# Performance work log

Measured on AMD Instinct MI355X. Metric: run time of the kernel, lower is better.

Reference implementation:

```python
import jax, jax.numpy as jnp
import numpy as np

OBS, ACT, EMB, DET, STO = 512, 32, 1024, 1024, 256
T, B = 64, 256
KL_SCALE = 1.0


def setup_inputs() -> dict:
    key = jax.random.key(0)
    ks = jax.random.split(key, 24)
    s = 0.02
    inp = {
        "obs": jax.random.normal(ks[0], (T, B, OBS), jnp.float32),
        "actions": jax.random.normal(ks[1], (T, B, ACT), jnp.float32),
        "rewards": jax.random.normal(ks[2], (T, B), jnp.float32),
        "dones": jnp.zeros((T, B), jnp.bool_),
        "eps": jax.random.normal(ks[3], (T - 1, B, STO), jnp.float32),
        # encoder: Linear(OBS,EMB) -> ReLU -> Linear(EMB,EMB) -> ReLU
        "enc_w1": jax.random.normal(ks[4], (OBS, EMB)) * s,
        "enc_b1": jnp.zeros((EMB,)),
        "enc_w2": jax.random.normal(ks[5], (EMB, EMB)) * s,
        "enc_b2": jnp.zeros((EMB,)),
        # GRUCell(STO+ACT, DET), torch layout [3*DET, in], gate order r,z,n
        "gru_wih": jax.random.normal(ks[6], (3 * DET, STO + ACT)) * s,
        "gru_whh": jax.random.normal(ks[7], (3 * DET, DET)) * s,
        "gru_bih": jnp.zeros((3 * DET,)),
        "gru_bhh": jnp.zeros((3 * DET,)),
        # prior / posterior nets
        "prior_w": jax.random.normal(ks[8], (DET, 2 * STO)) * s,
        "prior_b": jnp.zeros((2 * STO,)),
        "post_w": jax.random.normal(ks[9], (DET + EMB, 2 * STO)) * s,
        "post_b": jnp.zeros((2 * STO,)),
        # obs decoder
        "dec_w1": jax.random.normal(ks[10], (DET + STO, EMB)) * s,
        "dec_b1": jnp.zeros((EMB,)),
        "dec_w2": jax.random.normal(ks[11], (EMB, OBS)) * s,
        "dec_b2": jnp.zeros((OBS,)),
        # reward head
        "rew_w1": jax.random.normal(ks[12], (DET + STO, EMB)) * s,
        "rew_b1": jnp.zeros((EMB,)),
        "rew_w2": jax.random.normal(ks[13], (EMB, 1)) * s,
        "rew_b2": jnp.zeros((1,)),
    }
    return inp


def _kl(mq, lq, mp, lp):
    vq = jnp.exp(2.0 * lq)
    vp = jnp.exp(2.0 * lp)
    kl = lp - lq + (vq + (mq - mp) ** 2) / (vp + 1e-8) - 1.0
    return 0.5 * jnp.sum(kl, axis=-1)


def reference(obs, actions, rewards, dones, eps,
              enc_w1, enc_b1, enc_w2, enc_b2,
              gru_wih, gru_whh, gru_bih, gru_bhh,
              prior_w, prior_b, post_w, post_b,
              dec_w1, dec_b1, dec_w2, dec_b2,
              rew_w1, rew_b1, rew_w2, rew_b2):
    def step(carry, xs):
        h, z = carry
        o_t, o_next, a_t, r_t, d_t, e_t = xs
        # encoder
        emb = jax.nn.relu(jax.nn.relu(o_t @ enc_w1 + enc_b1) @ enc_w2 + enc_b2)
        # prior / posterior
        pm, pl = jnp.split(h @ prior_w + prior_b, 2, axis=-1)
        qm, ql = jnp.split(jnp.concatenate([h, emb], -1) @ post_w + post_b, 2, axis=-1)
        z_post = qm + e_t * jnp.exp(ql)
        # GRUCell (torch semantics)
        x = jnp.concatenate([z_post, a_t], -1)
        gi = x @ gru_wih.T + gru_bih
        gh = h @ gru_whh.T + gru_bhh
        ir, iz, inn = jnp.split(gi, 3, -1)
        hr, hz, hn = jnp.split(gh, 3, -1)
        r = jax.nn.sigmoid(ir + hr)
        u = jax.nn.sigmoid(iz + hz)
        n = jnp.tanh(inn + r * hn)
        h_next = (1.0 - u) * n + u * h
        feat = jnp.concatenate([h_next, z_post], -1)
        pred_obs = jax.nn.relu(feat @ dec_w1 + dec_b1) @ dec_w2 + dec_b2
        pred_rew = (jax.nn.relu(feat @ rew_w1 + rew_b1) @ rew_w2 + rew_b2)[..., 0]
        recon = jnp.mean((pred_obs - o_next) ** 2, axis=-1)  # [B]
        rew_l = (pred_rew - r_t) ** 2                         # [B]
        kl = _kl(qm, ql, pm, pl)                              # [B]
        mask = 1.0 - d_t.astype(h_next.dtype)[:, None]
        return (h_next * mask, z_post * mask), (recon, rew_l, kl)

    h0 = jnp.zeros((B, DET), obs.dtype)
    z0 = jnp.zeros((B, STO), obs.dtype)
    xs = (obs[:-1], obs[1:], actions[:-1], rewards[:-1], dones[:-1], eps)
    _, (recon, rew_l, kl) = jax.lax.scan(step, (h0, z0), xs)
    recon_loss = jnp.mean(recon)
    reward_loss = jnp.mean(rew_l)
    kl_loss = jnp.mean(kl)
    total = recon_loss + reward_loss + KL_SCALE * kl_loss
    return jnp.stack([total, recon_loss, reward_loss, kl_loss])
```

## Files before the change

kernel.cpp:

```cpp
#include <hip/hip_runtime.h>
#include <math.h>


namespace {

typedef unsigned short ushort;
typedef __attribute__((ext_vector_type(8))) short short8;
typedef __attribute__((ext_vector_type(4))) float f32x4;

constexpr int TSTEPS = 63;
constexpr int NB     = 256;
constexpr int NACT   = 32;
constexpr int NROWS  = TSTEPS * NB;
constexpr int TGRP   = 7;
constexpr int NGRP   = 9;
constexpr int GROWS  = TGRP * NB;

constexpr size_t OFF_POSTE = 0;
constexpr size_t OFF_OBSB  = OFF_POSTE + (size_t)NROWS * 512;
constexpr size_t OFF_E1C   = OFF_OBSB + (size_t)GROWS * 512 / 2;
constexpr size_t OFF_EMBC  = OFF_E1C + (size_t)GROWS * 1024 / 2;
constexpr size_t OFF_FEATC = OFF_EMBC + (size_t)GROWS * 1024 / 2;
constexpr size_t OFF_DR1C  = OFF_FEATC + (size_t)GROWS * 1280 / 2;
constexpr size_t OFF_WHT   = OFF_DR1C + (size_t)GROWS * 2048 / 2;
constexpr size_t OFF_WIHT  = OFF_WHT + (size_t)4096 * 1024 / 2;
constexpr size_t OFF_WDRT  = OFF_WIHT + (size_t)3072 * 288 / 2;
constexpr size_t OFF_E1T   = OFF_WDRT + (size_t)2048 * 1280 / 2;
constexpr size_t OFF_E2T   = OFF_E1T + (size_t)1024 * 512 / 2;
constexpr size_t OFF_PET   = OFF_E2T + (size_t)1024 * 1024 / 2;
constexpr size_t OFF_DW2T  = OFF_PET + (size_t)512 * 1024 / 2;
constexpr size_t OFF_BDR   = OFF_DW2T + (size_t)512 * 1024 / 2;
constexpr size_t OFF_G     = OFF_BDR + 2048;
constexpr size_t OFF_H     = OFF_G + (size_t)NB * 3072;
constexpr size_t OFF_HB    = OFF_H + (size_t)NB * 1024;
constexpr size_t OFF_ACC   = OFF_HB + (size_t)NB * 1024 / 2;
constexpr size_t OFF_XBUF  = OFF_ACC + 16;

__device__ __forceinline__ ushort f2bf(float f) {
  unsigned int u = __float_as_uint(f);
  unsigned int r = (u + 0x7fffu + ((u >> 16) & 1u)) >> 16;
  return (ushort)r;
}
__device__ __forceinline__ float bf2f(ushort u) {
  return __uint_as_float((unsigned int)u << 16);
}

__global__ void zero_kernel(float* p, int n) {
  int i = blockIdx.x * 256 + threadIdx.x;
  if (i < n) p[i] = 0.f;
}

__global__ void f2bf_kernel(const float* __restrict__ in, ushort* __restrict__ out, int n) {
  int i = blockIdx.x * 256 + threadIdx.x;
  if (i < n) out[i] = f2bf(in[i]);
}

__global__ void build_wht(const float* __restrict__ prior_w, const float* __restrict__ post_w,
                          const float* __restrict__ whh, ushort* __restrict__ out) {
  int idx = blockIdx.x * 256 + threadIdx.x;
  int n = idx >> 10, k = idx & 1023;
  float v;
  if (n < 1024) {
    int q = (n >> 4) & 3;
    int s = ((n >> 6) << 4) | (n & 15);
    v = (q == 0) ? prior_w[k * 512 + s]
      : (q == 1) ? prior_w[k * 512 + 256 + s]
      : (q == 2) ? post_w[k * 512 + s]
                 : post_w[k * 512 + 256 + s];
  } else {
    v = whh[(size_t)(n - 1024) * 1024 + k];
  }
  out[idx] = f2bf(v);
}

__global__ void trans_conv(const float* __restrict__ in, ushort* __restrict__ out,
                           int ldi, int ldo) {
  __shared__ float tile[32][33];
  int r0 = blockIdx.y * 32, c0 = blockIdx.x * 32;
  int tx = threadIdx.x & 31, ty = threadIdx.x >> 5;
#pragma unroll
  for (int p = 0; p < 4; ++p)
    tile[ty + p * 8][tx] = in[(size_t)(r0 + ty + p * 8) * ldi + c0 + tx];
  __syncthreads();
#pragma unroll
  for (int p = 0; p < 4; ++p)
    out[(size_t)(c0 + ty + p * 8) * ldo + r0 + tx] = f2bf(tile[tx][ty + p * 8]);
}

__global__ void build_bdr(const float* __restrict__ dec_b1, const float* __restrict__ rew_b1,
                          float* __restrict__ bdr) {
  int i = blockIdx.x * 256 + threadIdx.x;
  bdr[i] = (i < 1024) ? dec_b1[i] : rew_b1[i - 1024];
}

template <int EPI>
__global__ __launch_bounds__(256) void gemm_bf16(
    const ushort* __restrict__ A, const ushort* __restrict__ BT,
    const float* __restrict__ bias, void* __restrict__ Cv,
    int K, int lda, int ldb, int ldc) {
  __shared__ __align__(16) ushort As[64 * 40];
  __shared__ __align__(16) ushort Bs[64 * 40];
  int tid = threadIdx.x;
  int wave = tid >> 6, lane = tid & 63;
  int quad = lane >> 4, l15 = lane & 15;
  int m0 = blockIdx.y * 64, n0 = blockIdx.x * 64;
  int sr = tid >> 2, sc = (tid & 3) * 8;
  f32x4 acc[4] = {};
  for (int k0 = 0; k0 < K; k0 += 32) {
    *(int4*)&As[sr * 40 + sc] = *(const int4*)(A + (size_t)(m0 + sr) * lda + k0 + sc);
    *(int4*)&Bs[sr * 40 + sc] = *(const int4*)(BT + (size_t)(n0 + sr) * ldb + k0 + sc);
    __syncthreads();
    short8 a = *(const short8*)&As[(wave * 16 + l15) * 40 + quad * 8];
#pragma unroll
    for (int c = 0; c < 4; ++c) {
      short8 b = *(const short8*)&Bs[(c * 16 + l15) * 40 + quad * 8];
      acc[c] = __builtin_amdgcn_mfma_f32_16x16x32_bf16(a, b, acc[c], 0, 0, 0);
    }
    __syncthreads();
  }
#pragma unroll
  for (int c = 0; c < 4; ++c) {
#pragma unroll
    for (int r = 0; r < 4; ++r) {
      size_t row = m0 + wave * 16 + quad * 4 + r;
      int col = n0 + c * 16 + l15;
      float v = acc[c][r] + bias[col];
      if (EPI == 1) v = fmaxf(v, 0.f);
      if (EPI == 1) ((ushort*)Cv)[row * ldc + col] = f2bf(v);
      else ((float*)Cv)[row * ldc + col] = v;
    }
  }
}

__global__ __launch_bounds__(256) void step_g_kernel(
    int t, int tt, const ushort* __restrict__ HB, const ushort* __restrict__ WHT,
    const float* __restrict__ prior_b, const float* __restrict__ poste,
    const float* __restrict__ eps, const float* __restrict__ actions,
    float* __restrict__ G, ushort* __restrict__ xbuf,
    ushort* __restrict__ featc, float* __restrict__ acc_kl) {
  __shared__ __align__(16) ushort As[64 * 72];
  __shared__ __align__(16) ushort Bs[64 * 72];
  int tid = threadIdx.x;
  int wave = tid >> 6, lane = tid & 63;
  int quad = lane >> 4, l15 = lane & 15;
  int m0 = blockIdx.y * 64, n0 = blockIdx.x * 64;
  int sr = tid >> 2, sc = (tid & 3) * 16;
  const ushort* agp = HB + (size_t)(m0 + sr) * 1024 + sc;
  const ushort* bgp = WHT + (size_t)(n0 + sr) * 1024 + sc;
  int4 a0 = *(const int4*)agp, a1 = *(const int4*)(agp + 8);
  int4 b0 = *(const int4*)bgp, b1 = *(const int4*)(bgp + 8);
  f32x4 acc[4] = {};
  for (int k0 = 0;;) {
    *(int4*)&As[sr * 72 + sc] = a0; *(int4*)&As[sr * 72 + sc + 8] = a1;
    *(int4*)&Bs[sr * 72 + sc] = b0; *(int4*)&Bs[sr * 72 + sc + 8] = b1;
    __syncthreads();
    int kn = k0 + 64;
    if (kn < 1024) {
      a0 = *(const int4*)(agp + kn); a1 = *(const int4*)(agp + kn + 8);
      b0 = *(const int4*)(bgp + kn); b1 = *(const int4*)(bgp + kn + 8);
    }
#pragma unroll
    for (int kk = 0; kk < 2; ++kk) {
      short8 a = *(const short8*)&As[(wave * 16 + l15) * 72 + kk * 32 + quad * 8];
#pragma unroll
      for (int c = 0; c < 4; ++c) {
        short8 b = *(const short8*)&Bs[(c * 16 + l15) * 72 + kk * 32 + quad * 8];
        acc[c] = __builtin_amdgcn_mfma_f32_16x16x32_bf16(a, b, acc[c], 0, 0, 0);
      }
    }
    k0 = kn;
    if (k0 >= 1024) break;
    __syncthreads();
  }
  if (blockIdx.x < 16) {
    int s = (n0 >> 2) + l15;
    float kl_sum = 0.f;
#pragma unroll
    for (int r = 0; r < 4; ++r) {
      int b = m0 + wave * 16 + quad * 4 + r;
      size_t row = (size_t)t * NB + b;
      float pm = acc[0][r] + prior_b[s];
      float pl = acc[1][r] + prior_b[256 + s];
      float qm = acc[2][r] + poste[row * 512 + s];
      float ql = acc[3][r] + poste[row * 512 + 256 + s];
      float e = eps[row * 256 + s];
      float z = qm + e * expf(ql);
      xbuf[b * 288 + s] = f2bf(z);
      featc[(size_t)(tt * NB + b) * 1280 + 1024 + s] = f2bf(z);
      if (s < NACT) xbuf[b * 288 + 256 + s] = f2bf(actions[row * NACT + s]);
      float vq = expf(2.f * ql), vp = expf(2.f * pl);
      float dm = qm - pm;
      kl_sum += pl - ql + (vq + dm * dm) / (vp + 1e-8f) - 1.f;
    }
    for (int off = 32; off > 0; off >>= 1) kl_sum += __shfl_down(kl_sum, off);
    if (lane == 0) atomicAdd(acc_kl, 0.5f * kl_sum);
  } else {
    int ng = n0 - 1024;
#pragma unroll
    for (int c = 0; c < 4; ++c)
#pragma unroll
      for (int r = 0; r < 4; ++r) {
        int b = m0 + wave * 16 + quad * 4 + r;
        G[(size_t)b * 3072 + ng + c * 16 + l15] = acc[c][r];
      }
  }
}

__global__ __launch_bounds__(256) void gru_step_kernel(
    int t, int tt, const ushort* __restrict__ xbuf, const ushort* __restrict__ wiht,
    const float* __restrict__ G, const float* __restrict__ bih,
    const float* __restrict__ bhh, const unsigned char* __restrict__ dones,
    float* __restrict__ H, ushort* __restrict__ HB, ushort* __restrict__ featc) {
  __shared__ __align__(16) ushort As[64 * 40];
  __shared__ __align__(16) ushort Bs[3][64 * 40];
  int tid = threadIdx.x;
  int wave = tid >> 6, lane = tid & 63;
  int quad = lane >> 4, l15 = lane & 15;
  int m0 = blockIdx.y * 64, n0 = blockIdx.x * 64;
  int sr = tid >> 2, sc = (tid & 3) * 8;
  const ushort* agp = xbuf + (size_t)(m0 + sr) * 288 + sc;
  const ushort* bgp0 = wiht + (size_t)(n0 + sr) * 288 + sc;
  int4 pa = *(const int4*)agp;
  int4 pb0 = *(const int4*)bgp0;
  int4 pb1 = *(const int4*)(bgp0 + (size_t)1024 * 288);
  int4 pb2 = *(const int4*)(bgp0 + (size_t)2048 * 288);
  f32x4 accv[3][4] = {};
  for (int k0 = 0;;) {
    *(int4*)&As[sr * 40 + sc] = pa;
    *(int4*)&Bs[0][sr * 40 + sc] = pb0;
    *(int4*)&Bs[1][sr * 40 + sc] = pb1;
    *(int4*)&Bs[2][sr * 40 + sc] = pb2;
    __syncthreads();
    int kn = k0 + 32;
    if (kn < 288) {
      pa = *(const int4*)(agp + kn);
      pb0 = *(const int4*)(bgp0 + kn);
      pb1 = *(const int4*)(bgp0 + (size_t)1024 * 288 + kn);
      pb2 = *(const int4*)(bgp0 + (size_t)2048 * 288 + kn);
    }
    short8 a = *(const short8*)&As[(wave * 16 + l15) * 40 + quad * 8];
#pragma unroll
    for (int gg = 0; gg < 3; ++gg) {
#pragma unroll
      for (int c = 0; c < 4; ++c) {
        short8 b = *(const short8*)&Bs[gg][(c * 16 + l15) * 40 + quad * 8];
        accv[gg][c] = __builtin_amdgcn_mfma_f32_16x16x32_bf16(a, b, accv[gg][c], 0, 0, 0);
      }
    }
    k0 = kn;
    if (k0 >= 288) break;
    __syncthreads();
  }
#pragma unroll
  for (int c = 0; c < 4; ++c) {
#pragma unroll
    for (int r = 0; r < 4; ++r) {
      int b_idx = m0 + wave * 16 + quad * 4 + r;
      int j = n0 + c * 16 + l15;
      const float* g = G + (size_t)b_idx * 3072;
      float ir = accv[0][c][r] + bih[j];
      float iz = accv[1][c][r] + bih[1024 + j];
      float in_ = accv[2][c][r] + bih[2048 + j];
      float hr = g[j] + bhh[j];
      float hz = g[1024 + j] + bhh[1024 + j];
      float hn = g[2048 + j] + bhh[2048 + j];
      float rg = 1.f / (1.f + expf(-(ir + hr)));
      float u = 1.f / (1.f + expf(-(iz + hz)));
      float n = tanhf(in_ + rg * hn);
      float hprev = H[b_idx * 1024 + j];
      float hnext = (1.f - u) * n + u * hprev;
      featc[(size_t)(tt * NB + b_idx) * 1280 + j] = f2bf(hnext);
      float mask = 1.f - (float)dones[t * NB + b_idx];
      float hm = hnext * mask;
      H[b_idx * 1024 + j] = hm;
      HB[b_idx * 1024 + j] = f2bf(hm);
    }
  }
}

__global__ __launch_bounds__(256) void decobs_loss_kernel(
    const ushort* __restrict__ A, const ushort* __restrict__ BT,
    const float* __restrict__ bias, const float* __restrict__ obs_next_g,
    float* __restrict__ acc) {
  __shared__ __align__(16) ushort As[64 * 40];
  __shared__ __align__(16) ushort Bs[64 * 40];
  int tid = threadIdx.x;
  int wave = tid >> 6, lane = tid & 63;
  int quad = lane >> 4, l15 = lane & 15;
  int m0 = blockIdx.y * 64, n0 = blockIdx.x * 64;
  int sr = tid >> 2, sc = (tid & 3) * 8;
  f32x4 accm[4] = {};
  for (int k0 = 0; k0 < 1024; k0 += 32) {
    *(int4*)&As[sr * 40 + sc] = *(const int4*)(A + (size_t)(m0 + sr) * 2048 + k0 + sc);
    *(int4*)&Bs[sr * 40 + sc] = *(const int4*)(BT + (size_t)(n0 + sr) * 1024 + k0 + sc);
    __syncthreads();
    short8 a = *(const short8*)&As[(wave * 16 + l15) * 40 + quad * 8];
#pragma unroll
    for (int c = 0; c < 4; ++c) {
      short8 b = *(const short8*)&Bs[(c * 16 + l15) * 40 + quad * 8];
      accm[c] = __builtin_amdgcn_mfma_f32_16x16x32_bf16(a, b, accm[c], 0, 0, 0);
    }
    __syncthreads();
  }
  float local = 0.f;
#pragma unroll
  for (int c = 0; c < 4; ++c) {
#pragma unroll
    for (int r = 0; r < 4; ++r) {
      size_t row = m0 + wave * 16 + quad * 4 + r;
      int col = n0 + c * 16 + l15;
      float v = accm[c][r] + bias[col];
      float d = v - obs_next_g[row * 512 + col];
      local += d * d;
    }
  }
  __shared__ float red[256];
  red[tid] = local;
  __syncthreads();
  for (int st = 128; st > 0; st >>= 1) {
    if (tid < st) red[tid] += red[tid + st];
    __syncthreads();
  }
  if (tid == 0) atomicAdd(&acc[0], red[0]);
}

__global__ __launch_bounds__(256) void rew_loss_kernel(
    const ushort* __restrict__ R1, const float* __restrict__ w2,
    const float* __restrict__ b2, const float* __restrict__ rewards_g,
    float* __restrict__ acc) {
  int wave = threadIdx.x >> 6;
  int lane = threadIdx.x & 63;
  int row = blockIdx.x * 4 + wave;
  const ushort* rp = R1 + (size_t)row * 2048;
  float s = 0.f;
#pragma unroll
  for (int i = 0; i < 16; ++i) s += bf2f(rp[lane + 64 * i]) * w2[lane + 64 * i];
  for (int off = 32; off > 0; off >>= 1) s += __shfl_down(s, off);
  if (lane == 0) {
    float d = s + b2[0] - rewards_g[row];
    atomicAdd(&acc[1], d * d);
  }
}

__global__ void finalize_kernel(const float* __restrict__ acc, float* __restrict__ out) {
  float recon = acc[0] / ((float)NROWS * 512.f);
  float rew = acc[1] / (float)NROWS;
  float kl = acc[2] / (float)NROWS;
  out[0] = recon + rew + kl;
  out[1] = recon;
  out[2] = rew;
  out[3] = kl;
}

}

extern "C" void kernel_launch(void* const* d_in, const int* in_sizes, int n_in,
                              void* d_out, int out_size, void* d_ws, size_t ws_size,
                              hipStream_t stream) {
  const float* obs     = (const float*)d_in[0];
  const float* actions = (const float*)d_in[1];
  const float* rewards = (const float*)d_in[2];
  const unsigned char* dones = (const unsigned char*)d_in[3];
  const float* eps     = (const float*)d_in[4];
  const float* enc_w1  = (const float*)d_in[5];
  const float* enc_b1  = (const float*)d_in[6];
  const float* enc_w2  = (const float*)d_in[7];
  const float* enc_b2  = (const float*)d_in[8];
  const float* gru_wih = (const float*)d_in[9];
  const float* gru_whh = (const float*)d_in[10];
  const float* gru_bih = (const float*)d_in[11];
  const float* gru_bhh = (const float*)d_in[12];
  const float* prior_w = (const float*)d_in[13];
  const float* prior_b = (const float*)d_in[14];
  const float* post_w  = (const float*)d_in[15];
  const float* post_b  = (const float*)d_in[16];
  const float* dec_w1  = (const float*)d_in[17];
  const float* dec_b1  = (const float*)d_in[18];
  const float* dec_w2  = (const float*)d_in[19];
  const float* dec_b2  = (const float*)d_in[20];
  const float* rew_w1  = (const float*)d_in[21];
  const float* rew_b1  = (const float*)d_in[22];
  const float* rew_w2  = (const float*)d_in[23];
  const float* rew_b2  = (const float*)d_in[24];
  float* out = (float*)d_out;
  float* ws = (float*)d_ws;

  float*  POSTE = ws + OFF_POSTE;
  ushort* OBSB  = (ushort*)(ws + OFF_OBSB);
  ushort* E1C   = (ushort*)(ws + OFF_E1C);
  ushort* EMBC  = (ushort*)(ws + OFF_EMBC);
  ushort* FEATC = (ushort*)(ws + OFF_FEATC);
  ushort* DR1C  = (ushort*)(ws + OFF_DR1C);
  ushort* WHT   = (ushort*)(ws + OFF_WHT);
  ushort* WIHT  = (ushort*)(ws + OFF_WIHT);
  ushort* WDRT  = (ushort*)(ws + OFF_WDRT);
  ushort* E1T   = (ushort*)(ws + OFF_E1T);
  ushort* E2T   = (ushort*)(ws + OFF_E2T);
  ushort* PET   = (ushort*)(ws + OFF_PET);
  ushort* DW2T  = (ushort*)(ws + OFF_DW2T);
  float*  BDR   = ws + OFF_BDR;
  float*  G     = ws + OFF_G;
  float*  H     = ws + OFF_H;
  ushort* HB    = (ushort*)(ws + OFF_HB);
  float*  ACC   = ws + OFF_ACC;
  ushort* XBUF  = (ushort*)(ws + OFF_XBUF);

  {
    int nzero = NB * 1024 + NB * 512 + 16;
    zero_kernel<<<(nzero + 255) / 256, 256, 0, stream>>>(H, nzero);
  }
  build_wht<<<4096 * 1024 / 256, 256, 0, stream>>>(prior_w, post_w, gru_whh, WHT);
  f2bf_kernel<<<(3072 * 288) / 256, 256, 0, stream>>>(gru_wih, WIHT, 3072 * 288);
  trans_conv<<<dim3(1024 / 32, 1280 / 32), 256, 0, stream>>>(dec_w1, WDRT, 1024, 1280);
  trans_conv<<<dim3(1024 / 32, 1280 / 32), 256, 0, stream>>>(rew_w1, WDRT + (size_t)1024 * 1280, 1024, 1280);
  trans_conv<<<dim3(1024 / 32, 512 / 32), 256, 0, stream>>>(enc_w1, E1T, 1024, 512);
  trans_conv<<<dim3(1024 / 32, 1024 / 32), 256, 0, stream>>>(enc_w2, E2T, 1024, 1024);
  trans_conv<<<dim3(512 / 32, 1024 / 32), 256, 0, stream>>>(post_w + (size_t)1024 * 512, PET, 512, 1024);
  trans_conv<<<dim3(512 / 32, 1024 / 32), 256, 0, stream>>>(dec_w2, DW2T, 512, 1024);
  build_bdr<<<8, 256, 0, stream>>>(dec_b1, rew_b1, BDR);

  for (int g = 0; g < NGRP; ++g) {
    const float* obs_g = obs + (size_t)g * GROWS * 512;
    f2bf_kernel<<<(GROWS * 512) / 256, 256, 0, stream>>>(obs_g, OBSB, GROWS * 512);
    gemm_bf16<1><<<dim3(16, GROWS / 64), 256, 0, stream>>>(
        OBSB, E1T, enc_b1, E1C, 512, 512, 512, 1024);
    gemm_bf16<1><<<dim3(16, GROWS / 64), 256, 0, stream>>>(
        E1C, E2T, enc_b2, EMBC, 1024, 1024, 1024, 1024);
    gemm_bf16<2><<<dim3(8, GROWS / 64), 256, 0, stream>>>(
        EMBC, PET, post_b, POSTE + (size_t)g * GROWS * 512, 1024, 1024, 1024, 512);
  }

  for (int g = 0; g < NGRP; ++g) {
    for (int tt = 0; tt < TGRP; ++tt) {
      int t = g * TGRP + tt;
      step_g_kernel<<<dim3(64, 4), 256, 0, stream>>>(
          t, tt, HB, WHT, prior_b, POSTE, eps, actions, G, XBUF, FEATC, &ACC[2]);
      gru_step_kernel<<<dim3(16, 4), 256, 0, stream>>>(
          t, tt, XBUF, WIHT, G, gru_bih, gru_bhh, dones, H, HB, FEATC);
    }
    gemm_bf16<1><<<dim3(32, GROWS / 64), 256, 0, stream>>>(
        FEATC, WDRT, BDR, DR1C, 1280, 1280, 1280, 2048);
    decobs_loss_kernel<<<dim3(8, GROWS / 64), 256, 0, stream>>>(
        DR1C, DW2T, dec_b2, obs + ((size_t)g * TGRP + 1) * NB * 512, ACC);
    rew_loss_kernel<<<GROWS / 4, 256, 0, stream>>>(
        DR1C + 1024, rew_w2, rew_b2, rewards + (size_t)g * TGRP * NB, ACC);
  }

  finalize_kernel<<<1, 1, 0, stream>>>(ACC, out);
}
```

Measured before the change: 3.135 ms.

## Fuse recurrent step kernels into a cooperative persistent kernel with grid sync

Replaces the 126 per-timestep launches of the hidden-state GEMM and GRU update with one cooperative kernel per group of 7 timesteps. The two stages are separated by grid-wide barriers, and a fallback to the separate launches is kept if the cooperative launch fails. It also fuses the obs float-to-bf16 conversion into the first encoder GEMM, which drops a conversion kernel and its buffer. The aim is to remove launch overhead on the serial recurrence, at the cost of grid-sync latency and idle blocks during the GRU stage, where only 64 of 256 blocks work.

Measured after the change: 9.818 ms. 3.13x slower.

```diff
diff --git a/kernel.cpp b/kernel.cpp
--- a/kernel.cpp
+++ b/kernel.cpp
@@ -1,6 +1,9 @@
 #include <hip/hip_runtime.h>
+#include <hip/hip_cooperative_groups.h>
 #include <math.h>
 
+
+namespace cg = cooperative_groups;
 
 namespace {
 
@@ -17,8 +20,7 @@
 constexpr int GROWS  = TGRP * NB;
 
 constexpr size_t OFF_POSTE = 0;
-constexpr size_t OFF_OBSB  = OFF_POSTE + (size_t)NROWS * 512;
-constexpr size_t OFF_E1C   = OFF_OBSB + (size_t)GROWS * 512 / 2;
+constexpr size_t OFF_E1C   = OFF_POSTE + (size_t)NROWS * 512;
 constexpr size_t OFF_EMBC  = OFF_E1C + (size_t)GROWS * 1024 / 2;
 constexpr size_t OFF_FEATC = OFF_EMBC + (size_t)GROWS * 1024 / 2;
 constexpr size_t OFF_DR1C  = OFF_FEATC + (size_t)GROWS * 1280 / 2;
@@ -132,18 +134,59 @@
   }
 }
 
-__global__ __launch_bounds__(256) void step_g_kernel(
-    int t, int tt, const ushort* __restrict__ HB, const ushort* __restrict__ WHT,
+__global__ __launch_bounds__(256) void gemm_obs(
+    const float* __restrict__ A, const ushort* __restrict__ BT,
+    const float* __restrict__ bias, ushort* __restrict__ C) {
+  __shared__ __align__(16) ushort As[64 * 40];
+  __shared__ __align__(16) ushort Bs[64 * 40];
+  int tid = threadIdx.x;
+  int wave = tid >> 6, lane = tid & 63;
+  int quad = lane >> 4, l15 = lane & 15;
+  int m0 = blockIdx.y * 64, n0 = blockIdx.x * 64;
+  int sr = tid >> 2, sc = (tid & 3) * 8;
+  f32x4 acc[4] = {};
+  for (int k0 = 0; k0 < 512; k0 += 32) {
+    float4 f0 = *(const float4*)(A + (size_t)(m0 + sr) * 512 + k0 + sc);
+    float4 f1 = *(const float4*)(A + (size_t)(m0 + sr) * 512 + k0 + sc + 4);
+    union { int4 v; ushort u[8]; } cvt;
+    cvt.u[0] = f2bf(f0.x); cvt.u[1] = f2bf(f0.y); cvt.u[2] = f2bf(f0.z); cvt.u[3] = f2bf(f0.w);
+    cvt.u[4] = f2bf(f1.x); cvt.u[5] = f2bf(f1.y); cvt.u[6] = f2bf(f1.z); cvt.u[7] = f2bf(f1.w);
+    *(int4*)&As[sr * 40 + sc] = cvt.v;
+    *(int4*)&Bs[sr * 40 + sc] = *(const int4*)(BT + (size_t)(n0 + sr) * 512 + k0 + sc);
+    __syncthreads();
+    short8 a = *(const short8*)&As[(wave * 16 + l15) * 40 + quad * 8];
+#pragma unroll
+    for (int c = 0; c < 4; ++c) {
+      short8 b = *(const short8*)&Bs[(c * 16 + l15) * 40 + quad * 8];
+      acc[c] = __builtin_amdgcn_mfma_f32_16x16x32_bf16(a, b, acc[c], 0, 0, 0);
+    }
+    __syncthreads();
+  }
+#pragma unroll
+  for (int c = 0; c < 4; ++c) {
+#pragma unroll
+    for (int r = 0; r < 4; ++r) {
+      size_t row = m0 + wave * 16 + quad * 4 + r;
+      int col = n0 + c * 16 + l15;
+      float v = fmaxf(acc[c][r] + bias[col], 0.f);
+      C[row * 1024 + col] = f2bf(v);
+    }
+  }
+}
+
+__device__ __forceinline__ void stage_a_body(
+    int t, int tt, int bx, int by, ushort* smem,
+    const ushort* __restrict__ HB, const ushort* __restrict__ WHT,
     const float* __restrict__ prior_b, const float* __restrict__ poste,
     const float* __restrict__ eps, const float* __restrict__ actions,
     float* __restrict__ G, ushort* __restrict__ xbuf,
     ushort* __restrict__ featc, float* __restrict__ acc_kl) {
-  __shared__ __align__(16) ushort As[64 * 72];
-  __shared__ __align__(16) ushort Bs[64 * 72];
+  ushort* As = smem;
+  ushort* Bs = smem + 64 * 72;
   int tid = threadIdx.x;
   int wave = tid >> 6, lane = tid & 63;
   int quad = lane >> 4, l15 = lane & 15;
-  int m0 = blockIdx.y * 64, n0 = blockIdx.x * 64;
+  int m0 = by * 64, n0 = bx * 64;
   int sr = tid >> 2, sc = (tid & 3) * 16;
   const ushort* agp = HB + (size_t)(m0 + sr) * 1024 + sc;
   const ushort* bgp = WHT + (size_t)(n0 + sr) * 1024 + sc;
@@ -172,7 +215,7 @@
     if (k0 >= 1024) break;
     __syncthreads();
   }
-  if (blockIdx.x < 16) {
+  if (bx < 16) {
     int s = (n0 >> 2) + l15;
     float kl_sum = 0.f;
 #pragma unroll
@@ -206,46 +249,50 @@
   }
 }
 
-__global__ __launch_bounds__(256) void gru_step_kernel(
-    int t, int tt, const ushort* __restrict__ xbuf, const ushort* __restrict__ wiht,
+__device__ __forceinline__ void stage_b_body(
+    int t, int tt, int bx, int by, ushort* smem,
+    const ushort* __restrict__ xbuf, const ushort* __restrict__ WIHT,
     const float* __restrict__ G, const float* __restrict__ bih,
     const float* __restrict__ bhh, const unsigned char* __restrict__ dones,
     float* __restrict__ H, ushort* __restrict__ HB, ushort* __restrict__ featc) {
-  __shared__ __align__(16) ushort As[64 * 40];
-  __shared__ __align__(16) ushort Bs[3][64 * 40];
+  ushort* As  = smem;
+  ushort* Bs0 = smem + 2560;
+  ushort* Bs1 = smem + 2 * 2560;
+  ushort* Bs2 = smem + 3 * 2560;
   int tid = threadIdx.x;
   int wave = tid >> 6, lane = tid & 63;
   int quad = lane >> 4, l15 = lane & 15;
-  int m0 = blockIdx.y * 64, n0 = blockIdx.x * 64;
+  int m0 = by * 64, n0 = bx * 64;
   int sr = tid >> 2, sc = (tid & 3) * 8;
   const ushort* agp = xbuf + (size_t)(m0 + sr) * 288 + sc;
-  const ushort* bgp0 = wiht + (size_t)(n0 + sr) * 288 + sc;
+  const ushort* bgp0 = WIHT + (size_t)(n0 + sr) * 288 + sc;
   int4 pa = *(const int4*)agp;
   int4 pb0 = *(const int4*)bgp0;
   int4 pb1 = *(const int4*)(bgp0 + (size_t)1024 * 288);
   int4 pb2 = *(const int4*)(bgp0 + (size_t)2048 * 288);
   f32x4 accv[3][4] = {};
   for (int k0 = 0;;) {
-    *(int4*)&As[sr * 40 + sc] = pa;
-    *(int4*)&Bs[0][sr * 40 + sc] = pb0;
-    *(int4*)&Bs[1][sr * 40 + sc] = pb1;
-    *(int4*)&Bs[2][sr * 40 + sc] = pb2;
+    *(int4*)&As[sr * 40 + sc]  = pa;
+    *(int4*)&Bs0[sr * 40 + sc] = pb0;
+    *(int4*)&Bs1[sr * 40 + sc] = pb1;
+    *(int4*)&Bs2[sr * 40 + sc] = pb2;
     __syncthreads();
     int kn = k0 + 32;
     if (kn < 288) {
-      pa = *(const int4*)(agp + kn);
+      pa  = *(const int4*)(agp + kn);
       pb0 = *(const int4*)(bgp0 + kn);
       pb1 = *(const int4*)(bgp0 + (size_t)1024 * 288 + kn);
       pb2 = *(const int4*)(bgp0 + (size_t)2048 * 288 + kn);
     }
     short8 a = *(const short8*)&As[(wave * 16 + l15) * 40 + quad * 8];
 #pragma unroll
-    for (int gg = 0; gg < 3; ++gg) {
-#pragma unroll
-      for (int c = 0; c < 4; ++c) {
-        short8 b = *(const short8*)&Bs[gg][(c * 16 + l15) * 40 + quad * 8];
-        accv[gg][c] = __builtin_amdgcn_mfma_f32_16x16x32_bf16(a, b, accv[gg][c], 0, 0, 0);
-      }
+    for (int c = 0; c < 4; ++c) {
+      short8 b0v = *(const short8*)&Bs0[(c * 16 + l15) * 40 + quad * 8];
+      accv[0][c] = __builtin_amdgcn_mfma_f32_16x16x32_bf16(a, b0v, accv[0][c], 0, 0, 0);
+      short8 b1v = *(const short8*)&Bs1[(c * 16 + l15) * 40 + quad * 8];
+      accv[1][c] = __builtin_amdgcn_mfma_f32_16x16x32_bf16(a, b1v, accv[1][c], 0, 0, 0);
+      short8 b2v = *(const short8*)&Bs2[(c * 16 + l15) * 40 + quad * 8];
+      accv[2][c] = __builtin_amdgcn_mfma_f32_16x16x32_bf16(a, b2v, accv[2][c], 0, 0, 0);
     }
     k0 = kn;
     if (k0 >= 288) break;
@@ -257,13 +304,13 @@
     for (int r = 0; r < 4; ++r) {
       int b_idx = m0 + wave * 16 + quad * 4 + r;
       int j = n0 + c * 16 + l15;
-      const float* g = G + (size_t)b_idx * 3072;
+      const float* gp = G + (size_t)b_idx * 3072;
       float ir = accv[0][c][r] + bih[j];
       float iz = accv[1][c][r] + bih[1024 + j];
       float in_ = accv[2][c][r] + bih[2048 + j];
-      float hr = g[j] + bhh[j];
-      float hz = g[1024 + j] + bhh[1024 + j];
-      float hn = g[2048 + j] + bhh[2048 + j];
+      float hr = gp[j] + bhh[j];
+      float hz = gp[1024 + j] + bhh[1024 + j];
+      float hn = gp[2048 + j] + bhh[2048 + j];
       float rg = 1.f / (1.f + expf(-(ir + hr)));
       float u = 1.f / (1.f + expf(-(iz + hz)));
       float n = tanhf(in_ + rg * hn);
@@ -276,6 +323,53 @@
       HB[b_idx * 1024 + j] = f2bf(hm);
     }
   }
+}
+
+__global__ __launch_bounds__(256) void phase_b_group(
+    int g, const ushort* __restrict__ WHT, const ushort* __restrict__ WIHT,
+    const float* __restrict__ prior_b, const float* __restrict__ poste,
+    const float* __restrict__ eps, const float* __restrict__ actions,
+    const float* __restrict__ bih, const float* __restrict__ bhh,
+    const unsigned char* __restrict__ dones,
+    float* __restrict__ G, float* __restrict__ H, ushort* __restrict__ HB,
+    ushort* __restrict__ xbuf, ushort* __restrict__ featc,
+    float* __restrict__ acc_kl) {
+  cg::grid_group gridg = cg::this_grid();
+  __shared__ __align__(16) ushort smem[10240];
+  for (int tt = 0; tt < TGRP; ++tt) {
+    int t = g * TGRP + tt;
+    stage_a_body(t, tt, blockIdx.x & 63, blockIdx.x >> 6, smem,
+                 HB, WHT, prior_b, poste, eps, actions, G, xbuf, featc, acc_kl);
+    __threadfence();
+    gridg.sync();
+    if (blockIdx.x < 64) {
+      stage_b_body(t, tt, blockIdx.x & 15, blockIdx.x >> 4, smem,
+                   xbuf, WIHT, G, bih, bhh, dones, H, HB, featc);
+    }
+    __threadfence();
+    gridg.sync();
+  }
+}
+
+__global__ __launch_bounds__(256) void step_g_kernel(
+    int t, int tt, const ushort* __restrict__ HB, const ushort* __restrict__ WHT,
+    const float* __restrict__ prior_b, const float* __restrict__ poste,
+    const float* __restrict__ eps, const float* __restrict__ actions,
+    float* __restrict__ G, ushort* __restrict__ xbuf,
+    ushort* __restrict__ featc, float* __restrict__ acc_kl) {
+  __shared__ __align__(16) ushort smem[2 * 64 * 72];
+  stage_a_body(t, tt, blockIdx.x, blockIdx.y, smem,
+               HB, WHT, prior_b, poste, eps, actions, G, xbuf, featc, acc_kl);
+}
+
+__global__ __launch_bounds__(256) void gru_step_kernel(
+    int t, int tt, const ushort* __restrict__ xbuf, const ushort* __restrict__ WIHT,
+    const float* __restrict__ G, const float* __restrict__ bih,
+    const float* __restrict__ bhh, const unsigned char* __restrict__ dones,
+    float* __restrict__ H, ushort* __restrict__ HB, ushort* __restrict__ featc) {
+  __shared__ __align__(16) ushort smem[4 * 64 * 40];
+  stage_b_body(t, tt, blockIdx.x, blockIdx.y, smem,
+               xbuf, WIHT, G, bih, bhh, dones, H, HB, featc);
 }
 
 __global__ __launch_bounds__(256) void decobs_loss_kernel(
@@ -386,7 +480,6 @@
   float* ws = (float*)d_ws;
 
   float*  POSTE = ws + OFF_POSTE;
-  ushort* OBSB  = (ushort*)(ws + OFF_OBSB);
   ushort* E1C   = (ushort*)(ws + OFF_E1C);
   ushort* EMBC  = (ushort*)(ws + OFF_EMBC);
   ushort* FEATC = (ushort*)(ws + OFF_FEATC);
@@ -421,9 +514,7 @@
 
   for (int g = 0; g < NGRP; ++g) {
     const float* obs_g = obs + (size_t)g * GROWS * 512;
-    f2bf_kernel<<<(GROWS * 512) / 256, 256, 0, stream>>>(obs_g, OBSB, GROWS * 512);
-    gemm_bf16<1><<<dim3(16, GROWS / 64), 256, 0, stream>>>(
-        OBSB, E1T, enc_b1, E1C, 512, 512, 512, 1024);
+    gemm_obs<<<dim3(16, GROWS / 64), 256, 0, stream>>>(obs_g, E1T, enc_b1, E1C);
     gemm_bf16<1><<<dim3(16, GROWS / 64), 256, 0, stream>>>(
         E1C, E2T, enc_b2, EMBC, 1024, 1024, 1024, 1024);
     gemm_bf16<2><<<dim3(8, GROWS / 64), 256, 0, stream>>>(
@@ -431,12 +522,20 @@
   }
 
   for (int g = 0; g < NGRP; ++g) {
-    for (int tt = 0; tt < TGRP; ++tt) {
-      int t = g * TGRP + tt;
-      step_g_kernel<<<dim3(64, 4), 256, 0, stream>>>(
-          t, tt, HB, WHT, prior_b, POSTE, eps, actions, G, XBUF, FEATC, &ACC[2]);
-      gru_step_kernel<<<dim3(16, 4), 256, 0, stream>>>(
-          t, tt, XBUF, WIHT, G, gru_bih, gru_bhh, dones, H, HB, FEATC);
+    int garg = g;
+    float* acc_kl = &ACC[2];
+    void* args[] = {&garg, &WHT, &WIHT, &prior_b, &POSTE, &eps, &actions,
+                    &gru_bih, &gru_bhh, &dones, &G, &H, &HB, &XBUF, &FEATC, &acc_kl};
+    hipError_t cerr = hipLaunchCooperativeKernel(
+        (const void*)phase_b_group, dim3(256), dim3(256), args, 0, stream);
+    if (cerr != hipSuccess) {
+      for (int tt = 0; tt < TGRP; ++tt) {
+        int t = g * TGRP + tt;
+        step_g_kernel<<<dim3(64, 4), 256, 0, stream>>>(
+            t, tt, HB, WHT, prior_b, POSTE, eps, actions, G, XBUF, FEATC, &ACC[2]);
+        gru_step_kernel<<<dim3(16, 4), 256, 0, stream>>>(
+            t, tt, XBUF, WIHT, G, gru_bih, gru_bhh, dones, H, HB, FEATC);
+      }
     }
     gemm_bf16<1><<<dim3(32, GROWS / 64), 256, 0, stream>>>(
         FEATC, WDRT, BDR, DR1C, 1280, 1280, 1280, 2048);
```
